# Performance work log

Measured on AMD Instinct MI355X. Metric: run time of the kernel, lower is better.

The kernel has to match this reference:

```python
import jax, jax.numpy as jnp
import numpy as np

EPS = 1e-5
NEG = -1000000.0
H = 8

def layer_norm(v, g, b):
    mu = jnp.mean(v, axis=-1, keepdims=True)
    var = jnp.var(v, axis=-1, keepdims=True)
    return (v - mu) * jax.lax.rsqrt(var + EPS) * g + b

def setup_inputs() -> dict:
    key = jax.random.key(0)
    ks = jax.random.split(key, 12)
    B, T, Tc, D, Dc = 8, 2048, 512, 1024, 512
    s = lambda fan: 1.0 / np.sqrt(fan)
    return {
        'query': jax.random.normal(ks[0], (B, T, D), jnp.float32),
        'x': jax.random.normal(ks[1], (B, T, D), jnp.float32),
        'cond_emb': jax.random.normal(ks[2], (B, Tc, Dc), jnp.float32),
        'src_mask': jax.random.uniform(ks[3], (B, T, 1), jnp.float32),
        'cond_mask': jax.random.uniform(ks[4], (B, Tc, 1), jnp.float32),
        'norm_x_g': jnp.ones((D,), jnp.float32),
        'norm_x_b': jnp.zeros((D,), jnp.float32),
        'norm_c_g': jnp.ones((Dc,), jnp.float32),
        'norm_c_b': jnp.zeros((Dc,), jnp.float32),
        'W_kc': jax.random.normal(ks[5], (D, Dc), jnp.float32) * s(Dc),
        'b_kc': jnp.zeros((D,), jnp.float32),
        'W_vc': jax.random.normal(ks[6], (D, Dc), jnp.float32) * s(Dc),
        'b_vc': jnp.zeros((D,), jnp.float32),
        'W_kx': jax.random.normal(ks[7], (D, D), jnp.float32) * s(D),
        'b_kx': jnp.zeros((D,), jnp.float32),
        'W_vx': jax.random.normal(ks[8], (D, D), jnp.float32) * s(D),
        'b_vx': jnp.zeros((D,), jnp.float32),
        'W_y': jax.random.normal(ks[9], (D, D), jnp.float32) * s(D),
        'b_y': jnp.zeros((D,), jnp.float32),
    }

def reference(query, x, cond_emb, src_mask, cond_mask,
              norm_x_g, norm_x_b, norm_c_g, norm_c_b,
              W_kc, b_kc, W_vc, b_vc, W_kx, b_kx, W_vx, b_vx, W_y, b_y):
    B, T, D = x.shape
    Tc = cond_emb.shape[1]
    N = T + Tc
    xn = layer_norm(x, norm_x_g, norm_x_b)          # (B,T,D)
    cn = layer_norm(cond_emb, norm_c_g, norm_c_b)   # (B,Tc,Dc)
    # keys with additive mask penalty, concatenated over sequence dim
    k_cond = cn @ W_kc.T + b_kc + (1.0 - cond_mask) * NEG
    k_x = xn @ W_kx.T + b_kx + (1.0 - src_mask) * NEG
    key = jnp.concatenate([k_cond, k_x], axis=1)    # (B,N,D)
    q = jax.nn.softmax(query.reshape(B, T, H, D // H), axis=-1)
    k = jax.nn.softmax(key.reshape(B, N, H, D // H), axis=1)
    v_cond = (cn @ W_vc.T + b_vc) * cond_mask
    v_x = (xn @ W_vx.T + b_vx) * src_mask
    v = jnp.concatenate([v_cond, v_x], axis=1).reshape(B, N, H, D // H)
    attn = jnp.einsum('bnhd,bnhl->bhdl', k, v)      # (B,H,d,d) linear-attention KV
    y = jnp.einsum('bthd,bhdl->bthl', q, attn).reshape(B, T, D)
    return y @ W_y.T + b_y
```

## Files before the change

kernel.cpp:

```cpp
#include <hip/hip_runtime.h>


typedef short s16x8 __attribute__((ext_vector_type(8)));
typedef float f32x4 __attribute__((ext_vector_type(4)));

__device__ __forceinline__ float b2f(short s) {
    unsigned int u = ((unsigned int)(unsigned short)s) << 16;
    return __uint_as_float(u);
}
__device__ __forceinline__ short f2b(float f) {
    unsigned int u = __float_as_uint(f);
    u += 0x7fffu + ((u >> 16) & 1u);
    return (short)(u >> 16);
}

typedef void __attribute__((address_space(1)))* gas_ptr;
typedef void __attribute__((address_space(3)))* las_ptr;
__device__ __forceinline__ void async_cp16(const void* g, void* l) {
    __builtin_amdgcn_global_load_lds((gas_ptr)g, (las_ptr)l, 16, 0, 0);
}

__device__ __forceinline__ float pen_of(const float* __restrict__ cmask,
                                        const float* __restrict__ smask,
                                        int b, int n) {
    float mk = (n < 512) ? cmask[b * 512 + n] : smask[b * 2048 + n - 512];
    return (1.0f - mk) * -1000000.0f;
}

__device__ __forceinline__ void xcd_remap(int& gx, int& gy, int& gz) {
    int lb = blockIdx.x + gridDim.x * (blockIdx.y + gridDim.y * blockIdx.z);
    int nx = gridDim.x;
    int gpx = (gridDim.y * gridDim.z) >> 3;
    int xcd = lb & 7, rest = lb >> 3;
    gx = rest % nx;
    int gidx = xcd * gpx + rest / nx;
    gy = gidx % gridDim.y;
    gz = gidx / gridDim.y;
}

__global__ __launch_bounds__(256) void cvt_all(const float* __restrict__ Wkc,
                                               const float* __restrict__ Wvc,
                                               const float* __restrict__ Wkx,
                                               const float* __restrict__ Wvx,
                                               const float* __restrict__ Wy,
                                               short* __restrict__ dst) {
    int g = (blockIdx.x * 256 + threadIdx.x) * 4;
    const float* src;
    if (g < 524288)        src = Wkc + g;
    else if (g < 1048576)  src = Wvc + (g - 524288);
    else if (g < 2097152)  src = Wkx + (g - 1048576);
    else if (g < 3145728)  src = Wvx + (g - 2097152);
    else                   src = Wy  + (g - 3145728);
    float4 v = *(const float4*)src;
    short4 o;
    o.x = f2b(v.x); o.y = f2b(v.y); o.z = f2b(v.z); o.w = f2b(v.w);
    *(short4*)&dst[g] = o;
}

__global__ __launch_bounds__(256) void ln_kernel(const float* __restrict__ x,
                                                 const float* __restrict__ g,
                                                 const float* __restrict__ be,
                                                 short* __restrict__ out, int L) {
    long row = blockIdx.x;
    const float* xr = x + row * L;
    short* orow = out + row * L;
    int tid = threadIdx.x;
    int i0 = tid * 4;
    bool active = i0 < L;
    float v0 = 0.f, v1 = 0.f, v2 = 0.f, v3 = 0.f;
    if (active) {
        float4 p = *(const float4*)&xr[i0];
        v0 = p.x; v1 = p.y; v2 = p.z; v3 = p.w;
    }
    float s = v0 + v1 + v2 + v3;
    float s2 = v0*v0 + v1*v1 + v2*v2 + v3*v3;
    #pragma unroll
    for (int off = 32; off > 0; off >>= 1) {
        s  += __shfl_down(s, off);
        s2 += __shfl_down(s2, off);
    }
    __shared__ float ss[4], sq[4];
    int wave = tid >> 6, lane = tid & 63;
    if (lane == 0) { ss[wave] = s; sq[wave] = s2; }
    __syncthreads();
    if (tid == 0) {
        float t1 = ss[0] + ss[1] + ss[2] + ss[3];
        float t2 = sq[0] + sq[1] + sq[2] + sq[3];
        float mu = t1 / (float)L;
        float var = t2 / (float)L - mu * mu;
        ss[0] = mu;
        sq[0] = rsqrtf(var + 1e-5f);
    }
    __syncthreads();
    float mu = ss[0], rs = sq[0];
    if (active) {
        float4 gp = *(const float4*)&g[i0];
        float4 bp = *(const float4*)&be[i0];
        short4 o;
        o.x = f2b((v0 - mu) * rs * gp.x + bp.x);
        o.y = f2b((v1 - mu) * rs * gp.y + bp.y);
        o.z = f2b((v2 - mu) * rs * gp.z + bp.z);
        o.w = f2b((v3 - mu) * rs * gp.w + bp.w);
        *(short4*)&orow[i0] = o;
    }
}

__global__ __launch_bounds__(256) void qsoftmax_kernel(const float* __restrict__ q,
                                                       short* __restrict__ out) {
    long row = (long)blockIdx.x * 4 + (threadIdx.x >> 6);
    int lane = threadIdx.x & 63;
    const float* qr = q + row * 128;
    float2 p = *(const float2*)&qr[lane * 2];
    float v0 = p.x, v1 = p.y;
    float m = fmaxf(v0, v1);
    #pragma unroll
    for (int off = 32; off > 0; off >>= 1) m = fmaxf(m, __shfl_xor(m, off));
    float e0 = __expf(v0 - m), e1 = __expf(v1 - m);
    float s = e0 + e1;
    #pragma unroll
    for (int off = 32; off > 0; off >>= 1) s += __shfl_xor(s, off);
    float inv = 1.0f / s;
    short2 o; o.x = f2b(e0 * inv); o.y = f2b(e1 * inv);
    *(short2*)&out[row * 128 + lane * 2] = o;
}

__global__ __launch_bounds__(256) void kstats1(const short* __restrict__ klog,
                                               const float* __restrict__ cmask,
                                               const float* __restrict__ smask,
                                               float* __restrict__ partM,
                                               float* __restrict__ partS) {
    int c = blockIdx.x * 256 + threadIdx.x;
    int b = blockIdx.y;
    int n0 = blockIdx.z * 256;
    const short* base = klog + (long)b * 2560 * 1024 + c;
    float m = -3.4e38f, s = 0.f;
    for (int k = 0; k < 256; ++k) {
        int n = n0 + k;
        float v = b2f(base[(long)n * 1024]) + pen_of(cmask, smask, b, n);
        float nm = fmaxf(m, v);
        s = s * __expf(m - nm) + __expf(v - nm);
        m = nm;
    }
    long o = ((long)(b * 10 + blockIdx.z)) * 1024 + c;
    partM[o] = m;
    partS[o] = s;
}

__global__ __launch_bounds__(256) void kstats2(const float* __restrict__ partM,
                                               const float* __restrict__ partS,
                                               float* __restrict__ Ms,
                                               float* __restrict__ iSs) {
    int c = blockIdx.x * 256 + threadIdx.x;
    int b = blockIdx.y;
    float M = -3.4e38f;
    #pragma unroll
    for (int k = 0; k < 10; ++k)
        M = fmaxf(M, partM[((long)(b * 10 + k)) * 1024 + c]);
    float S = 0.f;
    #pragma unroll
    for (int k = 0; k < 10; ++k) {
        long o = ((long)(b * 10 + k)) * 1024 + c;
        S += partS[o] * __expf(partM[o] - M);
    }
    Ms[b * 1024 + c] = M;
    iSs[b * 1024 + c] = 1.0f / S;
}

template<int MODE>
__global__ __launch_bounds__(256) void gemm_bt(
        const short* __restrict__ A, int lda, long strideA,
        const short* __restrict__ B, int ldb,
        void* __restrict__ OutA, void* __restrict__ OutB,
        int ldo, long strideO,
        int K,
        const float* __restrict__ biasK, const float* __restrict__ biasV,
        const float* __restrict__ mask, long strideMask) {
    __shared__ short lds[4 * 8192];
    int tid = threadIdx.x;
    int wave = tid >> 6, lane = tid & 63;
    int bx, by, bz;
    xcd_remap(bx, by, bz);
    int n0 = bx * 128;
    int m0 = by * 128;
    int z = bz;

    const short* Ab;
    const short* Bb;
    if (MODE == 2) {
        Ab = A + (z & 7) * 128;
        Bb = B + (long)z * 16384;
    } else if (MODE == 4) {
        Ab = A + (long)z * strideA;
        Bb = B + (long)z * 1048576;
    } else {
        Ab = A + (long)z * strideA;
        Bb = B;
    }

    f32x4 acc[4][4];
    #pragma unroll
    for (int i = 0; i < 4; ++i)
        #pragma unroll
        for (int j = 0; j < 4; ++j) {
            f32x4 zz = {0.f, 0.f, 0.f, 0.f};
            acc[i][j] = zz;
        }

    int wm = wave >> 1, wn = wave & 1;
    int r = lane & 15, q = lane >> 4;

    const short* sp0; const short* sp1; const short* sp2; const short* sp3;
    int lo0, lo1, lo2, lo3;
    {
        #pragma unroll
        for (int it = 0; it < 4; ++it) {
            int cid = it * 256 + tid;
            int rid = cid & 511;
            int srow = rid >> 3;
            int scol = rid & 7;
            int scol0 = scol ^ (srow & 7);
            int row = srow * 2 + (scol0 >> 2);
            int col = (scol0 & 3) << 3;
            const short* p = (cid < 512)
                ? (Ab + (long)(m0 + row) * lda + col)
                : (Bb + (long)(n0 + row) * ldb + col);
            int lo = cid * 8;
            if (it == 0) { sp0 = p; lo0 = lo; }
            else if (it == 1) { sp1 = p; lo1 = lo; }
            else if (it == 2) { sp2 = p; lo2 = lo; }
            else { sp3 = p; lo3 = lo; }
        }
    }

    int offA[4], offB[4];
    #pragma unroll
    for (int i = 0; i < 4; ++i) {
        int rowA = wm * 64 + i * 16 + r;
        int srow = rowA >> 1;
        int slot = ((((rowA & 1) << 2) | q) ^ (srow & 7));
        offA[i] = srow * 64 + slot * 8;
        int rowB = wn * 64 + i * 16 + r;
        int srowB = rowB >> 1;
        int slotB = ((((rowB & 1) << 2) | q) ^ (srowB & 7));
        offB[i] = 4096 + srowB * 64 + slotB * 8;
    }

    int nt = K >> 5;
    #pragma unroll
    for (int pt = 0; pt < 3; ++pt) {
        async_cp16(sp0 + (pt << 5), &lds[pt * 8192 + lo0]);
        async_cp16(sp1 + (pt << 5), &lds[pt * 8192 + lo1]);
        async_cp16(sp2 + (pt << 5), &lds[pt * 8192 + lo2]);
        async_cp16(sp3 + (pt << 5), &lds[pt * 8192 + lo3]);
    }

    for (int t = 0; t < nt; ++t) {
        if (t + 2 < nt)
            asm volatile("s_waitcnt vmcnt(8)\n\ts_barrier" ::: "memory");
        else if (t + 1 < nt)
            asm volatile("s_waitcnt vmcnt(4)\n\ts_barrier" ::: "memory");
        else
            asm volatile("s_waitcnt vmcnt(0)\n\ts_barrier" ::: "memory");
        const short* base = &lds[(t & 3) * 8192];
        s16x8 af[4], bfr[4];
        #pragma unroll
        for (int j = 0; j < 4; ++j) bfr[j] = *(const s16x8*)&base[offB[j]];
        #pragma unroll
        for (int i = 0; i < 4; ++i) af[i] = *(const s16x8*)&base[offA[i]];
        if (t + 3 < nt) {
            int buf = (t + 3) & 3;
            int ks = (t + 3) << 5;
            async_cp16(sp0 + ks, &lds[buf * 8192 + lo0]);
            async_cp16(sp1 + ks, &lds[buf * 8192 + lo1]);
            async_cp16(sp2 + ks, &lds[buf * 8192 + lo2]);
            async_cp16(sp3 + ks, &lds[buf * 8192 + lo3]);
        }
        __builtin_amdgcn_s_setprio(1);
        #pragma unroll
        for (int i = 0; i < 4; ++i)
            #pragma unroll
            for (int j = 0; j < 4; ++j)
                acc[i][j] = __builtin_amdgcn_mfma_f32_16x16x32_bf16(af[i], bfr[j], acc[i][j], 0, 0, 0);
        __builtin_amdgcn_s_setprio(0);
    }

    #pragma unroll
    for (int i = 0; i < 4; ++i) {
        int gmb = m0 + wm * 64 + i * 16 + q * 4;
        #pragma unroll
        for (int j = 0; j < 4; ++j) {
            int gn = n0 + wn * 64 + j * 16 + r;
            #pragma unroll
            for (int rg = 0; rg < 4; ++rg) {
                int row = gmb + rg;
                float v = acc[i][j][rg];
                if (MODE == 0) {
                    if (gn < 1024) {
                        ((short*)OutA)[(long)z * strideO + (long)row * ldo + gn] =
                            f2b(v + biasK[gn]);
                    } else {
                        int gv = gn - 1024;
                        float mk = mask[(long)z * strideMask + row];
                        ((short*)OutB)[(long)z * strideO + (long)row * ldo + gv] =
                            f2b((v + biasV[gv]) * mk);
                    }
                } else if (MODE == 2) {
                    ((short*)OutA)[(long)(z >> 3) * 1048576 + (long)row * 1024 +
                                   (z & 7) * 128 + gn] = f2b(v);
                } else {
                    ((float*)OutA)[(long)z * strideO + (long)row * ldo + gn] =
                        v + biasK[gn];
                }
            }
        }
    }
}

template<int MODE>
__global__ __launch_bounds__(512, 2) void gemm256(
        const short* __restrict__ A, int lda, long strideA,
        const short* __restrict__ B, int ldb,
        void* __restrict__ OutA, void* __restrict__ OutB,
        int ldo, long strideO,
        int K,
        const float* __restrict__ biasK, const float* __restrict__ biasV,
        const float* __restrict__ mask, long strideMask) {
    extern __shared__ short lds[];
    int tid = threadIdx.x;
    int wave = tid >> 6, lane = tid & 63;
    int bx, by, bz;
    xcd_remap(bx, by, bz);
    int n0 = bx * 256;
    int m0 = by * 256;
    int z = bz;

    const short* Ab;
    const short* Bb;
    if (MODE == 4) {
        Ab = A + (long)z * strideA;
        Bb = B + (long)z * 1048576;
    } else {
        Ab = A + (long)z * strideA;
        Bb = B;
    }

    f32x4 acc[8][4];
    #pragma unroll
    for (int i = 0; i < 8; ++i)
        #pragma unroll
        for (int j = 0; j < 4; ++j) {
            f32x4 zz = {0.f, 0.f, 0.f, 0.f};
            acc[i][j] = zz;
        }

    int wm = wave >> 2, wn = wave & 3;
    int r = lane & 15, q = lane >> 4;

    const short* sp0; const short* sp1; const short* sp2; const short* sp3;
    int lo0, lo1, lo2, lo3;
    {
        #pragma unroll
        for (int it = 0; it < 4; ++it) {
            int cid = it * 512 + tid;
            int rid = cid & 1023;
            int srow = rid >> 3;
            int scol = rid & 7;
            int scol0 = scol ^ (srow & 7);
            int row = srow * 2 + (scol0 >> 2);
            int col = (scol0 & 3) << 3;
            const short* p = (cid < 1024)
                ? (Ab + (long)(m0 + row) * lda + col)
                : (Bb + (long)(n0 + row) * ldb + col);
            int lo = cid * 8;
            if (it == 0) { sp0 = p; lo0 = lo; }
            else if (it == 1) { sp1 = p; lo1 = lo; }
            else if (it == 2) { sp2 = p; lo2 = lo; }
            else { sp3 = p; lo3 = lo; }
        }
    }

    int offA[8], offB[4];
    #pragma unroll
    for (int i = 0; i < 8; ++i) {
        int rowA = wm * 128 + i * 16 + r;
        int srow = rowA >> 1;
        int slot = ((((rowA & 1) << 2) | q) ^ (srow & 7));
        offA[i] = srow * 64 + slot * 8;
    }
    #pragma unroll
    for (int j = 0; j < 4; ++j) {
        int rowB = wn * 64 + j * 16 + r;
        int srow = rowB >> 1;
        int slot = ((((rowB & 1) << 2) | q) ^ (srow & 7));
        offB[j] = 8192 + srow * 64 + slot * 8;
    }

    int nt = K >> 5;
    #pragma unroll
    for (int pt = 0; pt < 3; ++pt) {
        async_cp16(sp0 + (pt << 5), &lds[pt * 16384 + lo0]);
        async_cp16(sp1 + (pt << 5), &lds[pt * 16384 + lo1]);
        async_cp16(sp2 + (pt << 5), &lds[pt * 16384 + lo2]);
        async_cp16(sp3 + (pt << 5), &lds[pt * 16384 + lo3]);
    }

    for (int t = 0; t < nt; ++t) {
        if (t + 2 < nt)
            asm volatile("s_waitcnt vmcnt(8)\n\ts_barrier" ::: "memory");
        else if (t + 1 < nt)
            asm volatile("s_waitcnt vmcnt(4)\n\ts_barrier" ::: "memory");
        else
            asm volatile("s_waitcnt vmcnt(0)\n\ts_barrier" ::: "memory");
        const short* base = &lds[(t & 3) * 16384];
        s16x8 af[8], bfr[4];
        #pragma unroll
        for (int j = 0; j < 4; ++j) bfr[j] = *(const s16x8*)&base[offB[j]];
        #pragma unroll
        for (int i = 0; i < 8; ++i) af[i] = *(const s16x8*)&base[offA[i]];
        if (t + 3 < nt) {
            int buf = (t + 3) & 3;
            int ks = (t + 3) << 5;
            async_cp16(sp0 + ks, &lds[buf * 16384 + lo0]);
            async_cp16(sp1 + ks, &lds[buf * 16384 + lo1]);
            async_cp16(sp2 + ks, &lds[buf * 16384 + lo2]);
            async_cp16(sp3 + ks, &lds[buf * 16384 + lo3]);
        }
        __builtin_amdgcn_s_setprio(1);
        #pragma unroll
        for (int i = 0; i < 8; ++i)
            #pragma unroll
            for (int j = 0; j < 4; ++j)
                acc[i][j] = __builtin_amdgcn_mfma_f32_16x16x32_bf16(af[i], bfr[j], acc[i][j], 0, 0, 0);
        __builtin_amdgcn_s_setprio(0);
    }

    #pragma unroll
    for (int i = 0; i < 8; ++i) {
        int gmb = m0 + wm * 128 + i * 16 + q * 4;
        #pragma unroll
        for (int j = 0; j < 4; ++j) {
            int gn = n0 + wn * 64 + j * 16 + r;
            #pragma unroll
            for (int rg = 0; rg < 4; ++rg) {
                int row = gmb + rg;
                float v = acc[i][j][rg];
                if (MODE == 0) {
                    if (gn < 1024) {
                        ((short*)OutA)[(long)z * strideO + (long)row * ldo + gn] =
                            f2b(v + biasK[gn]);
                    } else {
                        int gv = gn - 1024;
                        float mk = mask[(long)z * strideMask + row];
                        ((short*)OutB)[(long)z * strideO + (long)row * ldo + gv] =
                            f2b((v + biasV[gv]) * mk);
                    }
                } else {
                    ((float*)OutA)[(long)z * strideO + (long)row * ldo + gn] =
                        v + biasK[gn];
                }
            }
        }
    }
}

__global__ __launch_bounds__(256) void attn_part(const short* __restrict__ klog,
                                                 const short* __restrict__ vbuf,
                                                 const float* __restrict__ cmask,
                                                 const float* __restrict__ smask,
                                                 const float* __restrict__ Ms,
                                                 float* __restrict__ pbuf) {
    __shared__ short kT[128 * 64];
    __shared__ short vT[128 * 64];
    int ns = blockIdx.x;
    int z = blockIdx.y;
    int b = z >> 3, h = z & 7;
    int tid = threadIdx.x;
    int wave = tid >> 6, lane = tid & 63;
    int r = lane & 15, q = lane >> 4;
    int wm = wave >> 1, wn = wave & 1;

    int cg = h * 128 + lane * 2;
    float M0 = Ms[b * 1024 + cg];
    float M1 = Ms[b * 1024 + cg + 1];

    f32x4 acc[4][4];
    #pragma unroll
    for (int i = 0; i < 4; ++i)
        #pragma unroll
        for (int j = 0; j < 4; ++j) {
            f32x4 zz = {0.f, 0.f, 0.f, 0.f};
            acc[i][j] = zz;
        }

    long base = ((long)b * 2560) * 1024 + h * 128;
    int nbase = ns * 320;
    int swz = (lane & 7) << 3;
    for (int n0 = 0; n0 < 320; n0 += 64) {
        __syncthreads();
        #pragma unroll 4
        for (int i = 0; i < 16; ++i) {
            int nl = i * 4 + wave;
            int n = nbase + n0 + nl;
            float pen = pen_of(cmask, smask, b, n);
            long g = base + (long)n * 1024 + lane * 2;
            short2 k2 = *(const short2*)&klog[g];
            short2 v2 = *(const short2*)&vbuf[g];
            float w0 = __expf(b2f(k2.x) + pen - M0);
            float w1 = __expf(b2f(k2.y) + pen - M1);
            int c = lane * 2;
            int sw = nl ^ swz;
            kT[c * 64 + sw] = f2b(w0);
            kT[(c + 1) * 64 + sw] = f2b(w1);
            vT[c * 64 + sw] = v2.x;
            vT[(c + 1) * 64 + sw] = v2.y;
        }
        __syncthreads();
        #pragma unroll
        for (int kk = 0; kk < 64; kk += 32) {
            s16x8 af[4], bfr[4];
            #pragma unroll
            for (int i = 0; i < 4; ++i) {
                int cA = wm * 64 + i * 16 + r;
                int cB = wn * 64 + i * 16 + r;
                af[i]  = *(const s16x8*)&kT[cA * 64 + ((kk + q * 8) ^ (((cA >> 1) & 7) << 3))];
                bfr[i] = *(const s16x8*)&vT[cB * 64 + ((kk + q * 8) ^ (((cB >> 1) & 7) << 3))];
            }
            #pragma unroll
            for (int i = 0; i < 4; ++i)
                #pragma unroll
                for (int j = 0; j < 4; ++j)
                    acc[i][j] = __builtin_amdgcn_mfma_f32_16x16x32_bf16(af[i], bfr[j], acc[i][j], 0, 0, 0);
        }
    }
    float* outp = pbuf + ((long)z * 8 + ns) * 16384;
    #pragma unroll
    for (int i = 0; i < 4; ++i) {
        int d0 = wm * 64 + i * 16 + q * 4;
        #pragma unroll
        for (int j = 0; j < 4; ++j) {
            int l = wn * 64 + j * 16 + r;
            *(f32x4*)&outp[l * 128 + d0] = acc[i][j];
        }
    }
}

__global__ __launch_bounds__(256) void reduce_attn(const float* __restrict__ pbuf,
                                                   const float* __restrict__ iSs,
                                                   short* __restrict__ attnD) {
    int idx = blockIdx.x * 256 + threadIdx.x;
    int z = idx >> 14, rem = idx & 16383;
    int d = rem & 127, l = rem >> 7;
    int b = z >> 3, h = z & 7;
    const float* p = pbuf + (long)z * 8 * 16384 + rem;
    float s = 0.f;
    #pragma unroll
    for (int ns = 0; ns < 8; ++ns) s += p[ns * 16384];
    attnD[(long)z * 16384 + d * 128 + l] = f2b(s * iSs[b * 1024 + h * 128 + d]);
}

extern "C" void kernel_launch(void* const* d_in, const int* in_sizes, int n_in,
                              void* d_out, int out_size, void* d_ws, size_t ws_size,
                              hipStream_t stream) {
    const float* query = (const float*)d_in[0];
    const float* x     = (const float*)d_in[1];
    const float* cond  = (const float*)d_in[2];
    const float* smask = (const float*)d_in[3];
    const float* cmask = (const float*)d_in[4];
    const float* gx  = (const float*)d_in[5];
    const float* bx  = (const float*)d_in[6];
    const float* gc  = (const float*)d_in[7];
    const float* bc  = (const float*)d_in[8];
    const float* Wkc = (const float*)d_in[9];
    const float* bkc = (const float*)d_in[10];
    const float* Wvc = (const float*)d_in[11];
    const float* bvc = (const float*)d_in[12];
    const float* Wkx = (const float*)d_in[13];
    const float* bkx = (const float*)d_in[14];
    const float* Wvx = (const float*)d_in[15];
    const float* bvx = (const float*)d_in[16];
    const float* Wy  = (const float*)d_in[17];
    const float* by  = (const float*)d_in[18];

    size_t o_xn    = 0;
    size_t o_cn    = o_xn    + 33554432;
    size_t o_klog  = o_cn    + 4194304;
    size_t o_vbuf  = o_klog  + 41943040;
    size_t o_qsm   = o_vbuf  + 41943040;
    size_t o_attnD = o_qsm   + 33554432;
    size_t o_partM = o_attnD + 2097152;
    size_t o_partS = o_partM + 327680;
    size_t o_Ms    = o_partS + 327680;
    size_t o_iSs   = o_Ms    + 32768;
    size_t o_wkc   = o_iSs   + 32768;
    size_t o_wvc   = o_wkc   + 1048576;
    size_t o_wkx   = o_wvc   + 1048576;
    size_t o_wvx   = o_wkx   + 2097152;
    size_t o_wy    = o_wvx   + 2097152;
    size_t need    = o_wy    + 2097152;
    if (ws_size < need) return;

    char* w = (char*)d_ws;
    short* xn    = (short*)(w + o_xn);
    short* cn    = (short*)(w + o_cn);
    short* klog  = (short*)(w + o_klog);
    short* vbuf  = (short*)(w + o_vbuf);
    short* qsm   = (short*)(w + o_qsm);
    short* attnD = (short*)(w + o_attnD);
    float* partM = (float*)(w + o_partM);
    float* partS = (float*)(w + o_partS);
    float* Ms    = (float*)(w + o_Ms);
    float* iSs   = (float*)(w + o_iSs);
    short* wkc   = (short*)(w + o_wkc);
    short* wkx   = (short*)(w + o_wkx);
    short* wy    = (short*)(w + o_wy);
    float* pbuf  = (float*)xn;
    short* Zt    = klog;

    static bool attr_set = false;
    if (!attr_set) {
        (void)hipFuncSetAttribute((const void*)gemm256<0>,
                                  hipFuncAttributeMaxDynamicSharedMemorySize, 131072);
        (void)hipFuncSetAttribute((const void*)gemm256<4>,
                                  hipFuncAttributeMaxDynamicSharedMemorySize, 131072);
        attr_set = true;
    }

    cvt_all<<<4096, 256, 0, stream>>>(Wkc, Wvc, Wkx, Wvx, Wy, wkc);

    ln_kernel<<<16384, 256, 0, stream>>>(x, gx, bx, xn, 1024);
    ln_kernel<<<4096, 256, 0, stream>>>(cond, gc, bc, cn, 512);
    qsoftmax_kernel<<<32768, 256, 0, stream>>>(query, qsm);

    gemm256<0><<<dim3(8, 8, 8), 512, 131072, stream>>>(
        xn, 1024, 2097152L, wkx, 1024,
        klog + 512 * 1024, vbuf + 512 * 1024, 1024, 2621440L,
        1024, bkx, bvx, smask, 2048L);
    gemm_bt<0><<<dim3(16, 4, 8), 256, 0, stream>>>(
        cn, 512, 262144L, wkc, 512,
        klog, vbuf, 1024, 2621440L,
        512, bkc, bvc, cmask, 512L);

    kstats1<<<dim3(4, 8, 10), 256, 0, stream>>>(klog, cmask, smask, partM, partS);
    kstats2<<<dim3(4, 8), 256, 0, stream>>>(partM, partS, Ms, iSs);

    attn_part<<<dim3(8, 64), 256, 0, stream>>>(klog, vbuf, cmask, smask, Ms, pbuf);
    reduce_attn<<<4096, 256, 0, stream>>>(pbuf, iSs, attnD);

    gemm_bt<2><<<dim3(1, 8, 64), 256, 0, stream>>>(
        wy, 1024, 0L, attnD, 128,
        Zt, nullptr, 1024, 0L,
        128, nullptr, nullptr, nullptr, 0L);
    gemm256<4><<<dim3(4, 8, 8), 512, 131072, stream>>>(
        qsm, 1024, 2097152L, Zt, 1024,
        d_out, nullptr, 1024, 2097152L,
        1024, by, nullptr, nullptr, 0L);
}
```

Measured before the change: 489.8 us.

## Restructure 256-tile GEMM main loop into four-phase ping-pong schedule

The 256x256 GEMM now steps K by 64 per iteration over two double-buffered LDS stages. Each iteration is split into four barrier-separated phases, each loading half the A or B fragments and issuing one async copy group for a future slice, interleaved with 16 MFMAs. Occupancy hint drops to one block per CU, and the cond-embedding GEMM now uses the 256 tile instead of the 128 kernel, whose now-unused modes are removed. The aim is finer overlap of global-to-LDS copies with MFMA work; the cost is many more barriers per K step and fewer resident blocks.

```diff
diff --git a/kernel.cpp b/kernel.cpp
--- a/kernel.cpp
+++ b/kernel.cpp
@@ -189,9 +189,6 @@
     if (MODE == 2) {
         Ab = A + (z & 7) * 128;
         Bb = B + (long)z * 16384;
-    } else if (MODE == 4) {
-        Ab = A + (long)z * strideA;
-        Bb = B + (long)z * 1048576;
     } else {
         Ab = A + (long)z * strideA;
         Bb = B;
@@ -294,17 +291,7 @@
             for (int rg = 0; rg < 4; ++rg) {
                 int row = gmb + rg;
                 float v = acc[i][j][rg];
-                if (MODE == 0) {
-                    if (gn < 1024) {
-                        ((short*)OutA)[(long)z * strideO + (long)row * ldo + gn] =
-                            f2b(v + biasK[gn]);
-                    } else {
-                        int gv = gn - 1024;
-                        float mk = mask[(long)z * strideMask + row];
-                        ((short*)OutB)[(long)z * strideO + (long)row * ldo + gv] =
-                            f2b((v + biasV[gv]) * mk);
-                    }
-                } else if (MODE == 2) {
+                if (MODE == 2) {
                     ((short*)OutA)[(long)(z >> 3) * 1048576 + (long)row * 1024 +
                                    (z & 7) * 128 + gn] = f2b(v);
                 } else {
@@ -317,7 +304,7 @@
 }
 
 template<int MODE>
-__global__ __launch_bounds__(512, 2) void gemm256(
+__global__ __launch_bounds__(512, 1) void gemm256(
         const short* __restrict__ A, int lda, long strideA,
         const short* __restrict__ B, int ldb,
         void* __restrict__ OutA, void* __restrict__ OutB,
@@ -356,82 +343,138 @@
     int wm = wave >> 2, wn = wave & 3;
     int r = lane & 15, q = lane >> 4;
 
-    const short* sp0; const short* sp1; const short* sp2; const short* sp3;
-    int lo0, lo1, lo2, lo3;
+    const short* spA0; const short* spA1; const short* spB0; const short* spB1;
+    int loA0, loA1, loB0, loB1;
     {
-        #pragma unroll
-        for (int it = 0; it < 4; ++it) {
-            int cid = it * 512 + tid;
-            int rid = cid & 1023;
-            int srow = rid >> 3;
-            int scol = rid & 7;
-            int scol0 = scol ^ (srow & 7);
-            int row = srow * 2 + (scol0 >> 2);
-            int col = (scol0 & 3) << 3;
-            const short* p = (cid < 1024)
-                ? (Ab + (long)(m0 + row) * lda + col)
-                : (Bb + (long)(n0 + row) * ldb + col);
-            int lo = cid * 8;
-            if (it == 0) { sp0 = p; lo0 = lo; }
-            else if (it == 1) { sp1 = p; lo1 = lo; }
-            else if (it == 2) { sp2 = p; lo2 = lo; }
-            else { sp3 = p; lo3 = lo; }
-        }
+        int rid0 = tid, rid1 = 512 + tid;
+        int srow = rid0 >> 3, scol0 = (rid0 & 7) ^ (srow & 7);
+        int row0 = srow * 2 + (scol0 >> 2), col0 = (scol0 & 3) << 3;
+        srow = rid1 >> 3; scol0 = (rid1 & 7) ^ (srow & 7);
+        int row1 = srow * 2 + (scol0 >> 2), col1 = (scol0 & 3) << 3;
+        spA0 = Ab + (long)(m0 + row0) * lda + col0;  loA0 = rid0 * 8;
+        spA1 = Ab + (long)(m0 + row1) * lda + col1;  loA1 = rid1 * 8;
+        spB0 = Bb + (long)(n0 + row0) * ldb + col0;  loB0 = rid0 * 8;
+        spB1 = Bb + (long)(n0 + row1) * ldb + col1;  loB1 = rid1 * 8;
     }
 
     int offA[8], offB[4];
     #pragma unroll
     for (int i = 0; i < 8; ++i) {
-        int rowA = wm * 128 + i * 16 + r;
-        int srow = rowA >> 1;
-        int slot = ((((rowA & 1) << 2) | q) ^ (srow & 7));
-        offA[i] = srow * 64 + slot * 8;
+        int row = wm * 128 + i * 16 + r;
+        int pr = row >> 1;
+        int slot = ((((row & 1) << 2) | q) ^ (pr & 7));
+        offA[i] = pr * 64 + slot * 8;
     }
     #pragma unroll
     for (int j = 0; j < 4; ++j) {
-        int rowB = wn * 64 + j * 16 + r;
-        int srow = rowB >> 1;
-        int slot = ((((rowB & 1) << 2) | q) ^ (srow & 7));
-        offB[j] = 8192 + srow * 64 + slot * 8;
-    }
-
-    int nt = K >> 5;
-    #pragma unroll
-    for (int pt = 0; pt < 3; ++pt) {
-        async_cp16(sp0 + (pt << 5), &lds[pt * 16384 + lo0]);
-        async_cp16(sp1 + (pt << 5), &lds[pt * 16384 + lo1]);
-        async_cp16(sp2 + (pt << 5), &lds[pt * 16384 + lo2]);
-        async_cp16(sp3 + (pt << 5), &lds[pt * 16384 + lo3]);
-    }
+        int row = wn * 64 + j * 16 + r;
+        int pr = row >> 1;
+        int slot = ((((row & 1) << 2) | q) ^ (pr & 7));
+        offB[j] = pr * 64 + slot * 8;
+    }
+
+    int nt = K >> 6;
+
+    async_cp16(spA0 +  0, &lds[0     + loA0]); async_cp16(spA1 +  0, &lds[0     + loA1]);
+    async_cp16(spB0 +  0, &lds[16384 + loB0]); async_cp16(spB1 +  0, &lds[16384 + loB1]);
+    async_cp16(spA0 + 32, &lds[8192  + loA0]); async_cp16(spA1 + 32, &lds[8192  + loA1]);
+    async_cp16(spB0 + 32, &lds[24576 + loB0]); async_cp16(spB1 + 32, &lds[24576 + loB1]);
+    async_cp16(spA0 + 64, &lds[32768 + loA0]); async_cp16(spA1 + 64, &lds[32768 + loA1]);
+    async_cp16(spB0 + 64, &lds[49152 + loB0]); async_cp16(spB1 + 64, &lds[49152 + loB1]);
+    asm volatile("s_waitcnt vmcnt(4)" ::: "memory");
+    __builtin_amdgcn_s_barrier();
 
     for (int t = 0; t < nt; ++t) {
-        if (t + 2 < nt)
-            asm volatile("s_waitcnt vmcnt(8)\n\ts_barrier" ::: "memory");
-        else if (t + 1 < nt)
-            asm volatile("s_waitcnt vmcnt(4)\n\ts_barrier" ::: "memory");
-        else
-            asm volatile("s_waitcnt vmcnt(0)\n\ts_barrier" ::: "memory");
-        const short* base = &lds[(t & 3) * 16384];
-        s16x8 af[8], bfr[4];
-        #pragma unroll
-        for (int j = 0; j < 4; ++j) bfr[j] = *(const s16x8*)&base[offB[j]];
-        #pragma unroll
-        for (int i = 0; i < 8; ++i) af[i] = *(const s16x8*)&base[offA[i]];
-        if (t + 3 < nt) {
-            int buf = (t + 3) & 3;
-            int ks = (t + 3) << 5;
-            async_cp16(sp0 + ks, &lds[buf * 16384 + lo0]);
-            async_cp16(sp1 + ks, &lds[buf * 16384 + lo1]);
-            async_cp16(sp2 + ks, &lds[buf * 16384 + lo2]);
-            async_cp16(sp3 + ks, &lds[buf * 16384 + lo3]);
-        }
+        int b = t & 1;
+        const short* Ar = lds + b * 32768;
+        const short* Br = Ar + 16384;
+        s16x8 a[4], bf[4];
+
+        #pragma unroll
+        for (int j = 0; j < 4; ++j) bf[j] = *(const s16x8*)&Br[offB[j]];
+        #pragma unroll
+        for (int i = 0; i < 4; ++i) a[i] = *(const s16x8*)&Ar[offA[i]];
+        if (t + 1 < nt) {
+            int kb = ((t + 1) << 6) + 32;
+            short* d = lds + (b ^ 1) * 32768 + 8192;
+            async_cp16(spA0 + kb, d + loA0);
+            async_cp16(spA1 + kb, d + loA1);
+        }
+        __builtin_amdgcn_s_barrier();
+        asm volatile("s_waitcnt lgkmcnt(0)" ::: "memory");
         __builtin_amdgcn_s_setprio(1);
         #pragma unroll
-        for (int i = 0; i < 8; ++i)
+        for (int i = 0; i < 4; ++i)
             #pragma unroll
             for (int j = 0; j < 4; ++j)
-                acc[i][j] = __builtin_amdgcn_mfma_f32_16x16x32_bf16(af[i], bfr[j], acc[i][j], 0, 0, 0);
+                acc[i][j] = __builtin_amdgcn_mfma_f32_16x16x32_bf16(a[i], bf[j], acc[i][j], 0, 0, 0);
         __builtin_amdgcn_s_setprio(0);
+        __builtin_amdgcn_s_barrier();
+
+        #pragma unroll
+        for (int i = 0; i < 4; ++i) a[i] = *(const s16x8*)&Ar[offA[4 + i]];
+        if (t + 1 < nt) {
+            int kb = ((t + 1) << 6) + 32;
+            short* d = lds + (b ^ 1) * 32768 + 24576;
+            async_cp16(spB0 + kb, d + loB0);
+            async_cp16(spB1 + kb, d + loB1);
+        }
+        __builtin_amdgcn_s_barrier();
+        asm volatile("s_waitcnt lgkmcnt(0)" ::: "memory");
+        __builtin_amdgcn_s_setprio(1);
+        #pragma unroll
+        for (int i = 0; i < 4; ++i)
+            #pragma unroll
+            for (int j = 0; j < 4; ++j)
+                acc[4 + i][j] = __builtin_amdgcn_mfma_f32_16x16x32_bf16(a[i], bf[j], acc[4 + i][j], 0, 0, 0);
+        __builtin_amdgcn_s_setprio(0);
+        __builtin_amdgcn_s_barrier();
+
+        #pragma unroll
+        for (int j = 0; j < 4; ++j) bf[j] = *(const s16x8*)&Br[8192 + offB[j]];
+        #pragma unroll
+        for (int i = 0; i < 4; ++i) a[i] = *(const s16x8*)&Ar[8192 + offA[i]];
+        if (t + 2 < nt) {
+            int kb = (t + 2) << 6;
+            short* d = lds + b * 32768;
+            async_cp16(spA0 + kb, d + loA0);
+            async_cp16(spA1 + kb, d + loA1);
+        }
+        __builtin_amdgcn_s_barrier();
+        asm volatile("s_waitcnt lgkmcnt(0)" ::: "memory");
+        __builtin_amdgcn_s_setprio(1);
+        #pragma unroll
+        for (int i = 0; i < 4; ++i)
+            #pragma unroll
+            for (int j = 0; j < 4; ++j)
+                acc[i][j] = __builtin_amdgcn_mfma_f32_16x16x32_bf16(a[i], bf[j], acc[i][j], 0, 0, 0);
+        __builtin_amdgcn_s_setprio(0);
+        __builtin_amdgcn_s_barrier();
+
+        #pragma unroll
+        for (int i = 0; i < 4; ++i) a[i] = *(const s16x8*)&Ar[8192 + offA[4 + i]];
+        if (t + 2 < nt) {
+            int kb = (t + 2) << 6;
+            short* d = lds + b * 32768 + 16384;
+            async_cp16(spB0 + kb, d + loB0);
+            async_cp16(spB1 + kb, d + loB1);
+        }
+        __builtin_amdgcn_s_barrier();
+        asm volatile("s_waitcnt lgkmcnt(0)" ::: "memory");
+        __builtin_amdgcn_s_setprio(1);
+        #pragma unroll
+        for (int i = 0; i < 4; ++i)
+            #pragma unroll
+            for (int j = 0; j < 4; ++j)
+                acc[4 + i][j] = __builtin_amdgcn_mfma_f32_16x16x32_bf16(a[i], bf[j], acc[4 + i][j], 0, 0, 0);
+        __builtin_amdgcn_s_setprio(0);
+        if (t + 1 < nt) {
+            if (t + 2 < nt)
+                asm volatile("s_waitcnt vmcnt(4)" ::: "memory");
+            else
+                asm volatile("s_waitcnt vmcnt(0)" ::: "memory");
+        }
+        __builtin_amdgcn_s_barrier();
     }
 
     #pragma unroll
@@ -635,7 +678,7 @@
         xn, 1024, 2097152L, wkx, 1024,
         klog + 512 * 1024, vbuf + 512 * 1024, 1024, 2621440L,
         1024, bkx, bvx, smask, 2048L);
-    gemm_bt<0><<<dim3(16, 4, 8), 256, 0, stream>>>(
+    gemm256<0><<<dim3(8, 2, 8), 512, 131072, stream>>>(
         cn, 512, 262144L, wkc, 512,
         klog, vbuf, 1024, 2621440L,
         512, bkc, bvc, cmask, 512L);
```

Result: slower. 512.6 us (+4.6%).

## Use low-LDS double-buffered 256x256 GEMM variant for x K/V projection

Applied to the files above, without the earlier changes.

Adds a new GEMM kernel that uses a 64 KB static LDS double buffer with K-step 32 and launch bounds allowing multiple blocks per CU, instead of the 128 KB dynamic-LDS variant. It uses it for the xn projection producing K and V. The aim is more blocks resident per CU so one block's memory latency can hide behind another's MFMA work, with setprio around the MFMA loop. In exchange each block has shallower prefetch and more barriers per K. Register pressure is also a risk under the tighter launch bound.

```diff
diff --git a/kernel.cpp b/kernel.cpp
--- a/kernel.cpp
+++ b/kernel.cpp
@@ -463,6 +463,148 @@
     }
 }
 
+template<int MODE>
+__global__ __launch_bounds__(512, 4) void gemm256tlp(
+        const short* __restrict__ A, int lda, long strideA,
+        const short* __restrict__ B, int ldb,
+        void* __restrict__ OutA, void* __restrict__ OutB,
+        int ldo, long strideO,
+        int K,
+        const float* __restrict__ biasK, const float* __restrict__ biasV,
+        const float* __restrict__ mask, long strideMask) {
+    __shared__ short lds[2 * 16384];
+    int tid = threadIdx.x;
+    int wave = tid >> 6, lane = tid & 63;
+    int bx, by, bz;
+    xcd_remap(bx, by, bz);
+    int n0 = bx * 256;
+    int m0 = by * 256;
+    int z = bz;
+
+    const short* Ab = A + (long)z * strideA;
+    const short* Bb;
+    if (MODE == 4) Bb = B + (long)z * 1048576;
+    else           Bb = B;
+
+    f32x4 acc[8][4];
+    #pragma unroll
+    for (int i = 0; i < 8; ++i)
+        #pragma unroll
+        for (int j = 0; j < 4; ++j) {
+            f32x4 zz = {0.f, 0.f, 0.f, 0.f};
+            acc[i][j] = zz;
+        }
+
+    int wm = wave >> 2, wn = wave & 3;
+    int r = lane & 15, q = lane >> 4;
+
+    const short* sp0; const short* sp1; const short* sp2; const short* sp3;
+    int lo0, lo1, lo2, lo3;
+    {
+        #pragma unroll
+        for (int it = 0; it < 4; ++it) {
+            int cid = it * 512 + tid;
+            int rid = cid & 1023;
+            int srow = rid >> 3;
+            int scol = rid & 7;
+            int scol0 = scol ^ (srow & 7);
+            int row = srow * 2 + (scol0 >> 2);
+            int col = (scol0 & 3) << 3;
+            const short* p = (cid < 1024)
+                ? (Ab + (long)(m0 + row) * lda + col)
+                : (Bb + (long)(n0 + row) * ldb + col);
+            int lo = cid * 8;
+            if (it == 0) { sp0 = p; lo0 = lo; }
+            else if (it == 1) { sp1 = p; lo1 = lo; }
+            else if (it == 2) { sp2 = p; lo2 = lo; }
+            else { sp3 = p; lo3 = lo; }
+        }
+    }
+
+    int offA[8], offB[4];
+    #pragma unroll
+    for (int i = 0; i < 8; ++i) {
+        int rowA = wm * 128 + i * 16 + r;
+        int srow = rowA >> 1;
+        int slot = ((((rowA & 1) << 2) | q) ^ (srow & 7));
+        offA[i] = srow * 64 + slot * 8;
+    }
+    #pragma unroll
+    for (int j = 0; j < 4; ++j) {
+        int rowB = wn * 64 + j * 16 + r;
+        int srow = rowB >> 1;
+        int slot = ((((rowB & 1) << 2) | q) ^ (srow & 7));
+        offB[j] = 8192 + srow * 64 + slot * 8;
+    }
+
+    int nt = K >> 5;
+    async_cp16(sp0 +  0, &lds[lo0]);
+    async_cp16(sp1 +  0, &lds[lo1]);
+    async_cp16(sp2 +  0, &lds[lo2]);
+    async_cp16(sp3 +  0, &lds[lo3]);
+    async_cp16(sp0 + 32, &lds[16384 + lo0]);
+    async_cp16(sp1 + 32, &lds[16384 + lo1]);
+    async_cp16(sp2 + 32, &lds[16384 + lo2]);
+    async_cp16(sp3 + 32, &lds[16384 + lo3]);
+
+    for (int t = 0; t < nt; ++t) {
+        if (t + 1 < nt)
+            asm volatile("s_waitcnt vmcnt(4)\n\ts_barrier" ::: "memory");
+        else
+            asm volatile("s_waitcnt vmcnt(0)\n\ts_barrier" ::: "memory");
+        const short* base = &lds[(t & 1) * 16384];
+        s16x8 af[8], bfr[4];
+        #pragma unroll
+        for (int j = 0; j < 4; ++j) bfr[j] = *(const s16x8*)&base[offB[j]];
+        #pragma unroll
+        for (int i = 0; i < 8; ++i) af[i] = *(const s16x8*)&base[offA[i]];
+        asm volatile("s_barrier" ::: "memory");
+        if (t + 2 < nt) {
+            int ks = (t + 2) << 5;
+            short* d = &lds[(t & 1) * 16384];
+            async_cp16(sp0 + ks, d + lo0);
+            async_cp16(sp1 + ks, d + lo1);
+            async_cp16(sp2 + ks, d + lo2);
+            async_cp16(sp3 + ks, d + lo3);
+        }
+        __builtin_amdgcn_s_setprio(1);
+        #pragma unroll
+        for (int i = 0; i < 8; ++i)
+            #pragma unroll
+            for (int j = 0; j < 4; ++j)
+                acc[i][j] = __builtin_amdgcn_mfma_f32_16x16x32_bf16(af[i], bfr[j], acc[i][j], 0, 0, 0);
+        __builtin_amdgcn_s_setprio(0);
+    }
+
+    #pragma unroll
+    for (int i = 0; i < 8; ++i) {
+        int gmb = m0 + wm * 128 + i * 16 + q * 4;
+        #pragma unroll
+        for (int j = 0; j < 4; ++j) {
+            int gn = n0 + wn * 64 + j * 16 + r;
+            #pragma unroll
+            for (int rg = 0; rg < 4; ++rg) {
+                int row = gmb + rg;
+                float v = acc[i][j][rg];
+                if (MODE == 0) {
+                    if (gn < 1024) {
+                        ((short*)OutA)[(long)z * strideO + (long)row * ldo + gn] =
+                            f2b(v + biasK[gn]);
+                    } else {
+                        int gv = gn - 1024;
+                        float mk = mask[(long)z * strideMask + row];
+                        ((short*)OutB)[(long)z * strideO + (long)row * ldo + gv] =
+                            f2b((v + biasV[gv]) * mk);
+                    }
+                } else {
+                    ((float*)OutA)[(long)z * strideO + (long)row * ldo + gn] =
+                        v + biasK[gn];
+                }
+            }
+        }
+    }
+}
+
 __global__ __launch_bounds__(256) void attn_part(const short* __restrict__ klog,
                                                  const short* __restrict__ vbuf,
                                                  const float* __restrict__ cmask,
@@ -618,8 +760,6 @@
 
     static bool attr_set = false;
     if (!attr_set) {
-        (void)hipFuncSetAttribute((const void*)gemm256<0>,
-                                  hipFuncAttributeMaxDynamicSharedMemorySize, 131072);
         (void)hipFuncSetAttribute((const void*)gemm256<4>,
                                   hipFuncAttributeMaxDynamicSharedMemorySize, 131072);
         attr_set = true;
@@ -631,7 +771,7 @@
     ln_kernel<<<4096, 256, 0, stream>>>(cond, gc, bc, cn, 512);
     qsoftmax_kernel<<<32768, 256, 0, stream>>>(query, qsm);
 
-    gemm256<0><<<dim3(8, 8, 8), 512, 131072, stream>>>(
+    gemm256tlp<0><<<dim3(8, 8, 8), 512, 0, stream>>>(
         xn, 1024, 2097152L, wkx, 1024,
         klog + 512 * 1024, vbuf + 512 * 1024, 1024, 2621440L,
         1024, bkx, bvx, smask, 2048L);
```

Result: slower. 1.084 ms (+121.2%).

## Widen key-stat reduction, vectorize attn_part staging, split x-projection GEMM

Applied to the files above, without the earlier changes.

The key column softmax statistics kernel now splits the sequence into 40 chunks of 64 rows instead of 10 chunks of 256, and uses four independent online max/sum chains per thread. This adds parallelism and shortens the serial dependency chain. The partial buffers move into the cn workspace region to make room for the larger partial arrays. attn_part now stages keys and values with 4-wide loads per lane, handling two rows per wave per iteration. The x-projection GEMM is launched as two half-sequence launches instead of one, which adds a launch and relies on correct offsets into the mask and outputs.

```diff
diff --git a/kernel.cpp b/kernel.cpp
--- a/kernel.cpp
+++ b/kernel.cpp
@@ -131,19 +131,29 @@
                                                float* __restrict__ partS) {
     int c = blockIdx.x * 256 + threadIdx.x;
     int b = blockIdx.y;
-    int n0 = blockIdx.z * 256;
+    int n0 = blockIdx.z * 64;
     const short* base = klog + (long)b * 2560 * 1024 + c;
-    float m = -3.4e38f, s = 0.f;
-    for (int k = 0; k < 256; ++k) {
-        int n = n0 + k;
-        float v = b2f(base[(long)n * 1024]) + pen_of(cmask, smask, b, n);
-        float nm = fmaxf(m, v);
-        s = s * __expf(m - nm) + __expf(v - nm);
-        m = nm;
-    }
-    long o = ((long)(b * 10 + blockIdx.z)) * 1024 + c;
-    partM[o] = m;
-    partS[o] = s;
+    float m0 = -3.4e38f, m1 = -3.4e38f, m2 = -3.4e38f, m3 = -3.4e38f;
+    float s0 = 0.f, s1 = 0.f, s2 = 0.f, s3 = 0.f;
+    #pragma unroll 4
+    for (int k = 0; k < 16; ++k) {
+        int n = n0 + k * 4;
+        float v0 = b2f(base[(long)(n + 0) * 1024]) + pen_of(cmask, smask, b, n + 0);
+        float v1 = b2f(base[(long)(n + 1) * 1024]) + pen_of(cmask, smask, b, n + 1);
+        float v2 = b2f(base[(long)(n + 2) * 1024]) + pen_of(cmask, smask, b, n + 2);
+        float v3 = b2f(base[(long)(n + 3) * 1024]) + pen_of(cmask, smask, b, n + 3);
+        float nm;
+        nm = fmaxf(m0, v0); s0 = s0 * __expf(m0 - nm) + __expf(v0 - nm); m0 = nm;
+        nm = fmaxf(m1, v1); s1 = s1 * __expf(m1 - nm) + __expf(v1 - nm); m1 = nm;
+        nm = fmaxf(m2, v2); s2 = s2 * __expf(m2 - nm) + __expf(v2 - nm); m2 = nm;
+        nm = fmaxf(m3, v3); s3 = s3 * __expf(m3 - nm) + __expf(v3 - nm); m3 = nm;
+    }
+    float M = fmaxf(fmaxf(m0, m1), fmaxf(m2, m3));
+    float S = s0 * __expf(m0 - M) + s1 * __expf(m1 - M) +
+              s2 * __expf(m2 - M) + s3 * __expf(m3 - M);
+    long o = ((long)(b * 40 + blockIdx.z)) * 1024 + c;
+    partM[o] = M;
+    partS[o] = S;
 }
 
 __global__ __launch_bounds__(256) void kstats2(const float* __restrict__ partM,
@@ -153,13 +163,13 @@
     int c = blockIdx.x * 256 + threadIdx.x;
     int b = blockIdx.y;
     float M = -3.4e38f;
-    #pragma unroll
-    for (int k = 0; k < 10; ++k)
-        M = fmaxf(M, partM[((long)(b * 10 + k)) * 1024 + c]);
+    #pragma unroll 8
+    for (int k = 0; k < 40; ++k)
+        M = fmaxf(M, partM[((long)(b * 40 + k)) * 1024 + c]);
     float S = 0.f;
-    #pragma unroll
-    for (int k = 0; k < 10; ++k) {
-        long o = ((long)(b * 10 + k)) * 1024 + c;
+    #pragma unroll 8
+    for (int k = 0; k < 40; ++k) {
+        long o = ((long)(b * 40 + k)) * 1024 + c;
         S += partS[o] * __expf(partM[o] - M);
     }
     Ms[b * 1024 + c] = M;
@@ -479,9 +489,9 @@
     int r = lane & 15, q = lane >> 4;
     int wm = wave >> 1, wn = wave & 1;
 
-    int cg = h * 128 + lane * 2;
-    float M0 = Ms[b * 1024 + cg];
-    float M1 = Ms[b * 1024 + cg + 1];
+    int l5 = lane & 31;
+    int c = l5 * 4;
+    float4 Mv = *(const float4*)&Ms[b * 1024 + h * 128 + c];
 
     f32x4 acc[4][4];
     #pragma unroll
@@ -494,25 +504,32 @@
 
     long base = ((long)b * 2560) * 1024 + h * 128;
     int nbase = ns * 320;
-    int swz = (lane & 7) << 3;
+    int sw0x = ((l5 * 2) & 7) << 3;
+    int sw1x = ((l5 * 2 + 1) & 7) << 3;
     for (int n0 = 0; n0 < 320; n0 += 64) {
         __syncthreads();
-        #pragma unroll 4
-        for (int i = 0; i < 16; ++i) {
-            int nl = i * 4 + wave;
+        #pragma unroll
+        for (int i = 0; i < 8; ++i) {
+            int nl = i * 8 + wave * 2 + (lane >> 5);
             int n = nbase + n0 + nl;
             float pen = pen_of(cmask, smask, b, n);
-            long g = base + (long)n * 1024 + lane * 2;
-            short2 k2 = *(const short2*)&klog[g];
-            short2 v2 = *(const short2*)&vbuf[g];
-            float w0 = __expf(b2f(k2.x) + pen - M0);
-            float w1 = __expf(b2f(k2.y) + pen - M1);
-            int c = lane * 2;
-            int sw = nl ^ swz;
-            kT[c * 64 + sw] = f2b(w0);
-            kT[(c + 1) * 64 + sw] = f2b(w1);
-            vT[c * 64 + sw] = v2.x;
-            vT[(c + 1) * 64 + sw] = v2.y;
+            long g = base + (long)n * 1024 + c;
+            short4 k4 = *(const short4*)&klog[g];
+            short4 v4 = *(const short4*)&vbuf[g];
+            float w0 = __expf(b2f(k4.x) + pen - Mv.x);
+            float w1 = __expf(b2f(k4.y) + pen - Mv.y);
+            float w2 = __expf(b2f(k4.z) + pen - Mv.z);
+            float w3 = __expf(b2f(k4.w) + pen - Mv.w);
+            int sw0 = nl ^ sw0x;
+            int sw1 = nl ^ sw1x;
+            kT[(c + 0) * 64 + sw0] = f2b(w0);
+            kT[(c + 1) * 64 + sw0] = f2b(w1);
+            kT[(c + 2) * 64 + sw1] = f2b(w2);
+            kT[(c + 3) * 64 + sw1] = f2b(w3);
+            vT[(c + 0) * 64 + sw0] = v4.x;
+            vT[(c + 1) * 64 + sw0] = v4.y;
+            vT[(c + 2) * 64 + sw1] = v4.z;
+            vT[(c + 3) * 64 + sw1] = v4.w;
         }
         __syncthreads();
         #pragma unroll
@@ -606,8 +623,6 @@
     short* vbuf  = (short*)(w + o_vbuf);
     short* qsm   = (short*)(w + o_qsm);
     short* attnD = (short*)(w + o_attnD);
-    float* partM = (float*)(w + o_partM);
-    float* partS = (float*)(w + o_partS);
     float* Ms    = (float*)(w + o_Ms);
     float* iSs   = (float*)(w + o_iSs);
     short* wkc   = (short*)(w + o_wkc);
@@ -615,6 +630,8 @@
     short* wy    = (short*)(w + o_wy);
     float* pbuf  = (float*)xn;
     short* Zt    = klog;
+    float* partM = (float*)(w + o_cn);
+    float* partS = (float*)(w + o_cn + 1310720);
 
     static bool attr_set = false;
     if (!attr_set) {
@@ -631,16 +648,20 @@
     ln_kernel<<<4096, 256, 0, stream>>>(cond, gc, bc, cn, 512);
     qsoftmax_kernel<<<32768, 256, 0, stream>>>(query, qsm);
 
-    gemm256<0><<<dim3(8, 8, 8), 512, 131072, stream>>>(
+    gemm256<0><<<dim3(8, 4, 8), 512, 131072, stream>>>(
         xn, 1024, 2097152L, wkx, 1024,
         klog + 512 * 1024, vbuf + 512 * 1024, 1024, 2621440L,
         1024, bkx, bvx, smask, 2048L);
+    gemm256<0><<<dim3(8, 4, 8), 512, 131072, stream>>>(
+        xn + 1048576, 1024, 2097152L, wkx, 1024,
+        klog + 512 * 1024 + 1048576, vbuf + 512 * 1024 + 1048576, 1024, 2621440L,
+        1024, bkx, bvx, smask + 1024, 2048L);
     gemm_bt<0><<<dim3(16, 4, 8), 256, 0, stream>>>(
         cn, 512, 262144L, wkc, 512,
         klog, vbuf, 1024, 2621440L,
         512, bkc, bvc, cmask, 512L);
 
-    kstats1<<<dim3(4, 8, 10), 256, 0, stream>>>(klog, cmask, smask, partM, partS);
+    kstats1<<<dim3(4, 8, 40), 256, 0, stream>>>(klog, cmask, smask, partM, partS);
     kstats2<<<dim3(4, 8), 256, 0, stream>>>(partM, partS, Ms, iSs);
 
     attn_part<<<dim3(8, 64), 256, 0, stream>>>(klog, vbuf, cmask, smask, Ms, pbuf);
```

Result: faster. 473.2 us (-3.4%).
